# Performance work log

Measured on AMD Instinct MI355X. Metric: run time of the kernel, lower is better.

Reference implementation:

```python
import jax, jax.numpy as jnp
import numpy as np

B, S, D, H = 4, 2048, 256, 8  # batch, seq (context=target), hidden_dim, n_heads


def setup_inputs() -> dict:
    key = jax.random.key(0)
    ks = jax.random.split(key, 12)
    sd = 1.0 / np.sqrt(D)          # torch Linear default init scale (uniform bound)
    sdo = 1.0 / np.sqrt(H * D)
    inp = {
        "k": jax.random.normal(ks[0], (B, S, D), jnp.float32),
        "v": jax.random.normal(ks[1], (B, S, D), jnp.float32),
        "q": jax.random.normal(ks[2], (B, S, D), jnp.float32),
        # Per-head projection weights, stacked over heads. Stored so y = x @ W + b.
        "Wk": jax.random.uniform(ks[3], (H, D, D), jnp.float32, -sd, sd),
        "bk": jax.random.uniform(ks[4], (H, D), jnp.float32, -sd, sd),
        "Wv": jax.random.uniform(ks[5], (H, D, D), jnp.float32, -sd, sd),
        "bv": jax.random.uniform(ks[6], (H, D), jnp.float32, -sd, sd),
        "Wq": jax.random.uniform(ks[7], (H, D, D), jnp.float32, -sd, sd),
        "bq": jax.random.uniform(ks[8], (H, D), jnp.float32, -sd, sd),
        # Final mixing Linear: input is heads interleaved as (hidden, head) flattened,
        # i.e. input index = hid * H + head (torch stack(dim=-1).view order).
        "Wo": jax.random.uniform(ks[9], (H * D, D), jnp.float32, -sdo, sdo),
        "bo": jax.random.uniform(ks[10], (D,), jnp.float32, -sdo, sdo),
    }
    return inp


def reference(k, v, q, Wk, bk, Wv, bv, Wq, bq, Wo, bo):
    # Per-head linear projections (batched over heads instead of a Python loop)
    k_ = jnp.einsum('bmd,hde->bhme', k, Wk) + bk[None, :, None, :]  # [B,H,S,D]
    v_ = jnp.einsum('bmd,hde->bhme', v, Wv) + bv[None, :, None, :]
    q_ = jnp.einsum('bnd,hde->bhne', q, Wq) + bq[None, :, None, :]
    scale = jnp.asarray(np.sqrt(D), k.dtype)
    # dot attention: scores[b,h,n,m] = <q_n, k_m> / sqrt(D); softmax over keys m
    scores = jnp.einsum('bhnd,bhmd->bhnm', q_, k_) / scale
    w = jax.nn.softmax(scores, axis=-1)
    rep = jnp.einsum('bhnm,bhmd->bhnd', w, v_)  # [B,H,S,D]
    # torch: stack(heads, dim=-1) -> [B,S,D,H], then view -> [B,S,D*H] (hid-major)
    outs = rep.transpose(0, 2, 3, 1).reshape(rep.shape[0], rep.shape[2], -1)
    return outs @ Wo + bo
```

## Files before the change

kernel.cpp:

```cpp
#include <hip/hip_runtime.h>

#define BB 4
#define SS 2048
#define DD 256
#define HH 8

typedef unsigned short u16;
typedef __attribute__((ext_vector_type(8))) short bf16x8;
typedef __attribute__((ext_vector_type(4))) float f32x4;
typedef __attribute__((ext_vector_type(16))) float f32x16;
typedef __attribute__((ext_vector_type(4))) short s16x4;

__device__ __forceinline__ f32x4 MFMA(bf16x8 a, bf16x8 b, f32x4 c) {
    return __builtin_amdgcn_mfma_f32_16x16x32_bf16(a, b, c, 0, 0, 0);
}
__device__ __forceinline__ f32x16 MFMA32(bf16x8 a, bf16x8 b, f32x16 c) {
    return __builtin_amdgcn_mfma_f32_32x32x16_bf16(a, b, c, 0, 0, 0);
}

__device__ __forceinline__ u16 f2bf_rtn(float x) {
    unsigned u = __float_as_uint(x);
    u += 0x7FFFu + ((u >> 16) & 1u);
    return (u16)(u >> 16);
}
__device__ __forceinline__ float bf2f(u16 h) {
    return __uint_as_float(((unsigned)h) << 16);
}
__device__ __forceinline__ void split2(float x, u16 &hi, u16 &lo) {
    hi = f2bf_rtn(x);
    lo = f2bf_rtn(x - bf2f(hi));
}

__device__ __forceinline__ void gl_lds16(const u16* g, u16* l) {
    __builtin_amdgcn_global_load_lds(
        (const __attribute__((address_space(1))) unsigned int*)(g),
        (__attribute__((address_space(3))) unsigned int*)(l), 16, 0, 0);
}

__global__ void prep_a(const float* __restrict__ x, u16* __restrict__ hi) {
    int r = blockIdx.x;
    int d = threadIdx.x;
    hi[(size_t)r * 256 + d] = f2bf_rtn(x[(size_t)r * 256 + d]);
}

__global__ void prep_w(const float* __restrict__ W, u16* __restrict__ Whi,
                       u16* __restrict__ Wlo) {
    int n = blockIdx.x;
    int h = n >> 8, e = n & 255;
    int d = threadIdx.x;
    float x = W[((size_t)h * 256 + d) * 256 + e];
    u16 hi, lo; split2(x, hi, lo);
    Whi[(size_t)n * 256 + d] = hi;
    Wlo[(size_t)n * 256 + d] = lo;
}

__global__ void prep_wo(const float* __restrict__ W, u16* __restrict__ Whi,
                        u16* __restrict__ Wlo) {
    int n = blockIdx.x;
    for (int k = threadIdx.x; k < 2048; k += 256) {
        int d = k & 255, h = k >> 8;
        float x = W[((size_t)(d * 8 + h)) * 256 + n];
        u16 hi, lo; split2(x, hi, lo);
        Whi[(size_t)n * 2048 + k] = hi;
        Wlo[(size_t)n * 2048 + k] = lo;
    }
}

template<int MODE, int AMODE, int TERMS, int BN>
__global__ __launch_bounds__(512, 2) void gemm_split(
    const u16* __restrict__ Ahi, const u16* __restrict__ Alo,
    const u16* __restrict__ Bhi, const u16* __restrict__ Blo,
    const float* __restrict__ bias,
    u16* __restrict__ Ohi,
    float* __restrict__ Of,
    int M, int N, int K, float scale)
{
    constexpr int WN = (BN == 128) ? 4 : 2;
    constexpr int WM = 8 / WN;
    constexpr int MSUB = (128 / WM) / 16;
    constexpr int NSUB = (BN / WN) / 16;
    constexpr int NPL = (TERMS == 3) ? 4 : (TERMS == 2) ? 3 : 2;

    __shared__ u16 lds[3 * NPL * 4096];

    const int tid = threadIdx.x;
    const int lane = tid & 63, wave = tid >> 6;
    const int wm = wave / WN, wn = wave % WN;
    const int m0 = blockIdx.y * 128, n0 = blockIdx.x * BN;

    f32x4 acc[MSUB][NSUB];
#pragma unroll
    for (int i = 0; i < MSUB; ++i)
#pragma unroll
        for (int j = 0; j < NSUB; ++j) acc[i][j] = {0.f, 0.f, 0.f, 0.f};

    const int rho = tid >> 2;
    const int Xs = (tid & 3) << 3;
    const int ldsW = wave * 512;

#define G_ISSUE(k0v, p)                                                         \
    {   u16* Bse = lds + (p) * (NPL * 4096);                                    \
        size_t ga;                                                              \
        if (AMODE == 0)                                                         \
            ga = (size_t)(m0 + rho) * K + (k0v) + Xs;                           \
        else                                                                    \
            ga = ((size_t)((m0 >> 11) * 8 + ((k0v) >> 8)) * SS                  \
                  + (m0 & 2047) + rho) * DD + ((k0v) & 255) + Xs;               \
        gl_lds16(Ahi + ga, Bse + ldsW);                                         \
        if (TERMS == 3) gl_lds16(Alo + ga, Bse + 3 * 4096 + ldsW);              \
        if (BN == 128 || tid < 256) {                                           \
            size_t gb = (size_t)(n0 + rho) * K + (k0v) + Xs;                    \
            gl_lds16(Bhi + gb, Bse + 1 * 4096 + ldsW);                          \
            if (TERMS >= 2) gl_lds16(Blo + gb, Bse + 2 * 4096 + ldsW);          \
        }                                                                       \
    }

    const int NK = K >> 5;
    G_ISSUE(0, 0);
    G_ISSUE(32, 1);

    int buf = 0;
    for (int kt = 0; kt < NK; ++kt) {
        if (kt < NK - 1) {
            if (TERMS == 1)      { asm volatile("s_waitcnt vmcnt(2)" ::: "memory"); }
            else if (TERMS == 2) { asm volatile("s_waitcnt vmcnt(3)" ::: "memory"); }
            else {
                if (wave < 4) { asm volatile("s_waitcnt vmcnt(4)" ::: "memory"); }
                else          { asm volatile("s_waitcnt vmcnt(2)" ::: "memory"); }
            }
        } else {
            asm volatile("s_waitcnt vmcnt(0)" ::: "memory");
        }
        __builtin_amdgcn_sched_barrier(0);
        __builtin_amdgcn_s_barrier();
        __builtin_amdgcn_sched_barrier(0);

        if (kt + 2 < NK) {
            const int p2 = (buf + 2 >= 3) ? buf - 1 : buf + 2;
            G_ISSUE((kt + 2) << 5, p2);
        }

        const u16* Bse = lds + buf * (NPL * 4096);
        const int g8 = (lane >> 4) << 3;
        const int rA = wm * (128 / WM), rB = wn * (BN / WN);
        bf16x8 bh[NSUB], bl[NSUB];
#pragma unroll
        for (int ns = 0; ns < NSUB; ++ns) {
            const int rb = rB + ns * 16 + (lane & 15);
            bh[ns] = *(const bf16x8*)(Bse + 1 * 4096 + rb * 32 + g8);
            if (TERMS >= 2) bl[ns] = *(const bf16x8*)(Bse + 2 * 4096 + rb * 32 + g8);
        }
#pragma unroll
        for (int ms = 0; ms < MSUB; ++ms) {
            const int ra = rA + ms * 16 + (lane & 15);
            bf16x8 ah = *(const bf16x8*)(Bse + ra * 32 + g8);
            bf16x8 al;
            if (TERMS == 3) al = *(const bf16x8*)(Bse + 3 * 4096 + ra * 32 + g8);
#pragma unroll
            for (int ns = 0; ns < NSUB; ++ns) {
                acc[ms][ns] = MFMA(ah, bh[ns], acc[ms][ns]);
                if (TERMS == 3) acc[ms][ns] = MFMA(al, bh[ns], acc[ms][ns]);
                if (TERMS >= 2) acc[ms][ns] = MFMA(ah, bl[ns], acc[ms][ns]);
            }
        }
        buf = (buf + 1 == 3) ? 0 : buf + 1;
    }
#undef G_ISSUE

#pragma unroll
    for (int ms = 0; ms < MSUB; ++ms)
#pragma unroll
        for (int ns = 0; ns < NSUB; ++ns)
#pragma unroll
            for (int r = 0; r < 4; ++r) {
                int row = m0 + wm * (128 / WM) + ms * 16 + (lane >> 4) * 4 + r;
                int col = n0 + wn * (BN / WN) + ns * 16 + (lane & 15);
                float v = (acc[ms][ns][r] + bias[col]) * scale;
                if (MODE == 2) {
                    Of[(size_t)row * N + col] = v;
                } else {
                    int b = row >> 11, s = row & 2047, hh = col >> 8, e = col & 255;
                    size_t idx;
                    if (MODE == 0)
                        idx = ((size_t)(b * HH + hh) * SS + s) * DD + e;
                    else
                        idx = ((size_t)(b * HH + hh) * DD + e) * SS + s;
                    Ohi[idx] = f2bf_rtn(v);
                }
            }
}

__global__ __launch_bounds__(512, 2) void attn_kernel(
    const u16* __restrict__ Qhi,
    const u16* __restrict__ Khi,
    const u16* __restrict__ Vhi,
    u16* __restrict__ Rhi, u16* __restrict__ Rlo)
{
    __shared__ u16 lK[3][8192];
    __shared__ u16 lV[3][8192];

    const int tid = threadIdx.x, lane = tid & 63, wave = tid >> 6;
    const int qc = lane & 31, g2 = lane >> 5;
    const int wg = ((blockIdx.x & 7) << 5) + (blockIdx.x >> 3);
    const int bh = wg >> 3;
    const int qt = wg & 7;
    const size_t base = (size_t)bh * SS * DD;
    const int q0w = qt * 256 + wave * 32;

    bf16x8 qB[16];
#pragma unroll
    for (int ks = 0; ks < 16; ++ks)
        qB[ks] = *(const bf16x8*)(Qhi + base + (size_t)(q0w + qc) * DD + ks * 16 + g2 * 8);

    int koff[2], voff[2];
#pragma unroll
    for (int i = 0; i < 2; ++i) {
        const int s = tid + i * 512;
        const int kr = s >> 5, kX = s & 31;
        const int kap = (kr & 0x13) | ((kr & 4) << 1) | ((kr & 8) >> 1);
        koff[i] = kap * DD + ((kX ^ kr) << 3);
        const int ve = s >> 2, vXs = s & 3;
        voff[i] = ve * SS + (((vXs ^ ((ve >> 3) & 3))) << 3);
    }

    float l_part = 0.f;
    f32x16 acc[8];
#pragma unroll
    for (int ec = 0; ec < 8; ++ec) acc[ec] = {};

#define ISSUE(tt, p)                                                            \
    {   const u16* Kg = Khi + base + (size_t)(tt) * 32 * DD;                    \
        const u16* Vg = Vhi + base + (size_t)(tt) * 32;                         \
        u16* Kb = &lK[p][0]; u16* Vb = &lV[p][0];                               \
        gl_lds16(Kg + koff[0], Kb + wave * 512);                                \
        gl_lds16(Kg + koff[1], Kb + wave * 512 + 4096);                         \
        gl_lds16(Vg + voff[0], Vb + wave * 512);                                \
        gl_lds16(Vg + voff[1], Vb + wave * 512 + 4096);                         \
    }

    ISSUE(0, 0);
    ISSUE(1, 1);

    for (int t = 0; t < 64; ++t) {
        if (t < 63) { asm volatile("s_waitcnt vmcnt(4)" ::: "memory"); }
        else        { asm volatile("s_waitcnt vmcnt(0)" ::: "memory"); }
        __builtin_amdgcn_sched_barrier(0);
        __builtin_amdgcn_s_barrier();
        __builtin_amdgcn_sched_barrier(0);

        if (t + 2 < 64) ISSUE(t + 2, (t + 2) % 3);

        const u16* Kb = &lK[t % 3][0];
        const u16* Vb = &lV[t % 3][0];

        f32x16 sa = {}, sb = {};
        __builtin_amdgcn_s_setprio(1);
#pragma unroll
        for (int ks = 0; ks < 8; ++ks) {
            bf16x8 ka = *(const bf16x8*)(Kb + qc * DD + (((2 * ks + g2) ^ qc) << 3));
            bf16x8 kb2 = *(const bf16x8*)(Kb + qc * DD + (((2 * (ks + 8) + g2) ^ qc) << 3));
            sa = MFMA32(ka, qB[ks], sa);
            sb = MFMA32(kb2, qB[ks + 8], sb);
        }
        __builtin_amdgcn_s_setprio(0);

        f32x16 s = sa + sb;
#pragma unroll
        for (int n = 0; n < 16; ++n) s[n] = __builtin_amdgcn_exp2f(s[n] - 8.0f);
        float tl = 0.f;
#pragma unroll
        for (int n = 0; n < 16; ++n) tl += s[n];
        l_part += tl;

        bf16x8 p0, p1;
#pragma unroll
        for (int j = 0; j < 8; ++j) p0[j] = (short)f2bf_rtn(s[j]);
#pragma unroll
        for (int j = 0; j < 8; ++j) p1[j] = (short)f2bf_rtn(s[8 + j]);

        __builtin_amdgcn_s_setprio(1);
#pragma unroll
        for (int ec = 0; ec < 8; ++ec) {
            const int e = ec * 32 + qc;
            bf16x8 v0 = *(const bf16x8*)(Vb + e * 32 + (((g2 ^ ((e >> 3) & 3))) << 3));
            bf16x8 v1 = *(const bf16x8*)(Vb + e * 32 + ((((2 + g2) ^ ((e >> 3) & 3))) << 3));
            acc[ec] = MFMA32(v0, p0, acc[ec]);
            acc[ec] = MFMA32(v1, p1, acc[ec]);
        }
        __builtin_amdgcn_s_setprio(0);
    }
#undef ISSUE

    float l = l_part + __shfl_xor(l_part, 32);
    float inv = 1.0f / l;
    const size_t rowbase = ((size_t)bh * SS + q0w + qc) * DD;
#pragma unroll
    for (int ec = 0; ec < 8; ++ec)
#pragma unroll
        for (int rr = 0; rr < 4; ++rr) {
            const int e0 = ec * 32 + 8 * rr + 4 * g2;
            s16x4 hv, lv;
#pragma unroll
            for (int j = 0; j < 4; ++j) {
                u16 h2, l2; split2(acc[ec][4 * rr + j] * inv, h2, l2);
                hv[j] = (short)h2; lv[j] = (short)l2;
            }
            *(s16x4*)(Rhi + rowbase + e0) = hv;
            *(s16x4*)(Rlo + rowbase + e0) = lv;
        }
}

extern "C" void kernel_launch(void* const* d_in, const int* in_sizes, int n_in,
                              void* d_out, int out_size, void* d_ws, size_t ws_size,
                              hipStream_t stream)
{
    (void)in_sizes; (void)n_in; (void)out_size; (void)ws_size;
    const float* k_in = (const float*)d_in[0];
    const float* v_in = (const float*)d_in[1];
    const float* q_in = (const float*)d_in[2];
    const float* Wk   = (const float*)d_in[3];
    const float* bk   = (const float*)d_in[4];
    const float* Wv   = (const float*)d_in[5];
    const float* bv   = (const float*)d_in[6];
    const float* Wq   = (const float*)d_in[7];
    const float* bq   = (const float*)d_in[8];
    const float* Wo   = (const float*)d_in[9];
    const float* bo   = (const float*)d_in[10];
    float* out = (float*)d_out;

    char* p = (char*)d_ws;
    const size_t MB = 1024 * 1024;
    u16* WqH = (u16*)(p + 0 * MB);
    u16* WqL = (u16*)(p + 1 * MB);
    u16* WkH = (u16*)(p + 2 * MB);
    u16* WkL = (u16*)(p + 3 * MB);
    u16* WvH = (u16*)(p + 4 * MB);
    u16* WvL = (u16*)(p + 5 * MB);
    u16* WoH = (u16*)(p + 6 * MB);
    u16* WoL = (u16*)(p + 7 * MB);
    const size_t PB = 32 * MB;
    u16* QH  = (u16*)(p + 8 * MB);
    u16* KH  = (u16*)(p + 8 * MB + 1 * PB);
    u16* VTH = (u16*)(p + 8 * MB + 2 * PB);
    u16* RH  = (u16*)(p + 8 * MB + 3 * PB);
    u16* RL  = (u16*)(p + 8 * MB + 4 * PB);
    u16* AqH = (u16*)(p + 168 * MB);
    u16* AkH = (u16*)(p + 172 * MB);
    u16* AvH = (u16*)(p + 176 * MB);

    prep_a<<<dim3(8192), dim3(256), 0, stream>>>(q_in, AqH);
    prep_a<<<dim3(8192), dim3(256), 0, stream>>>(k_in, AkH);
    prep_a<<<dim3(8192), dim3(256), 0, stream>>>(v_in, AvH);
    prep_w<<<dim3(2048), dim3(256), 0, stream>>>(Wq, WqH, WqL);
    prep_w<<<dim3(2048), dim3(256), 0, stream>>>(Wk, WkH, WkL);
    prep_w<<<dim3(2048), dim3(256), 0, stream>>>(Wv, WvH, WvL);
    prep_wo<<<dim3(256), dim3(256), 0, stream>>>(Wo, WoH, WoL);

    const float qscale = 1.4426950408889634f / 16.0f;
    gemm_split<0, 0, 1, 128><<<dim3(16, 64), dim3(512), 0, stream>>>(
        AqH, nullptr, WqH, WqL, bq, QH, nullptr, 8192, 2048, 256, qscale);
    gemm_split<0, 0, 1, 128><<<dim3(16, 64), dim3(512), 0, stream>>>(
        AkH, nullptr, WkH, WkL, bk, KH, nullptr, 8192, 2048, 256, 1.0f);
    gemm_split<1, 0, 2, 128><<<dim3(16, 64), dim3(512), 0, stream>>>(
        AvH, nullptr, WvH, WvL, bv, VTH, nullptr, 8192, 2048, 256, 1.0f);

    attn_kernel<<<dim3(256), dim3(512), 0, stream>>>(
        QH, KH, VTH, RH, RL);

    gemm_split<2, 2, 3, 64><<<dim3(4, 64), dim3(512), 0, stream>>>(
        RH, RL, WoH, WoL, bo, nullptr, out, 8192, 256, 2048, 1.0f);
}
```

Baseline: 309.6 us.

## Halve attention workgroup size to double grid, remap GEMM blocks XCD-aware

```diff
diff --git a/kernel.cpp b/kernel.cpp
--- a/kernel.cpp
+++ b/kernel.cpp
@@ -66,7 +66,7 @@
     }
 }
 
-template<int MODE, int AMODE, int TERMS, int BN>
+template<int MODE, int AMODE, int TERMS, int BN, int LNXB>
 __global__ __launch_bounds__(512, 2) void gemm_split(
     const u16* __restrict__ Ahi, const u16* __restrict__ Alo,
     const u16* __restrict__ Bhi, const u16* __restrict__ Blo,
@@ -86,7 +86,10 @@
     const int tid = threadIdx.x;
     const int lane = tid & 63, wave = tid >> 6;
     const int wm = wave / WN, wn = wave % WN;
-    const int m0 = blockIdx.y * 128, n0 = blockIdx.x * BN;
+    const int cpx = (int)gridDim.x >> 3;
+    const int wgs = (blockIdx.x & 7) * cpx + (blockIdx.x >> 3);
+    const int m0 = (wgs >> LNXB) * 128;
+    const int n0 = (wgs & ((1 << LNXB) - 1)) * BN;
 
     f32x4 acc[MSUB][NSUB];
 #pragma unroll
@@ -190,32 +193,32 @@
             }
 }
 
-__global__ __launch_bounds__(512, 2) void attn_kernel(
+__global__ __launch_bounds__(256, 2) void attn_kernel(
     const u16* __restrict__ Qhi,
     const u16* __restrict__ Khi,
     const u16* __restrict__ Vhi,
     u16* __restrict__ Rhi, u16* __restrict__ Rlo)
 {
-    __shared__ u16 lK[3][8192];
-    __shared__ u16 lV[3][8192];
+    __shared__ u16 lK[2][8192];
+    __shared__ u16 lV[2][8192];
 
     const int tid = threadIdx.x, lane = tid & 63, wave = tid >> 6;
     const int qc = lane & 31, g2 = lane >> 5;
-    const int wg = ((blockIdx.x & 7) << 5) + (blockIdx.x >> 3);
-    const int bh = wg >> 3;
-    const int qt = wg & 7;
+    const int wg = ((blockIdx.x & 7) << 6) + (blockIdx.x >> 3);
+    const int bh = wg >> 4;
+    const int qt = wg & 15;
     const size_t base = (size_t)bh * SS * DD;
-    const int q0w = qt * 256 + wave * 32;
+    const int q0w = qt * 128 + wave * 32;
 
     bf16x8 qB[16];
 #pragma unroll
     for (int ks = 0; ks < 16; ++ks)
         qB[ks] = *(const bf16x8*)(Qhi + base + (size_t)(q0w + qc) * DD + ks * 16 + g2 * 8);
 
-    int koff[2], voff[2];
-#pragma unroll
-    for (int i = 0; i < 2; ++i) {
-        const int s = tid + i * 512;
+    int koff[4], voff[4];
+#pragma unroll
+    for (int i = 0; i < 4; ++i) {
+        const int s = wave * 256 + i * 64 + lane;
         const int kr = s >> 5, kX = s & 31;
         const int kap = (kr & 0x13) | ((kr & 4) << 1) | ((kr & 8) >> 1);
         koff[i] = kap * DD + ((kX ^ kr) << 3);
@@ -231,27 +234,26 @@
 #define ISSUE(tt, p)                                                            \
     {   const u16* Kg = Khi + base + (size_t)(tt) * 32 * DD;                    \
         const u16* Vg = Vhi + base + (size_t)(tt) * 32;                         \
-        u16* Kb = &lK[p][0]; u16* Vb = &lV[p][0];                               \
-        gl_lds16(Kg + koff[0], Kb + wave * 512);                                \
-        gl_lds16(Kg + koff[1], Kb + wave * 512 + 4096);                         \
-        gl_lds16(Vg + voff[0], Vb + wave * 512);                                \
-        gl_lds16(Vg + voff[1], Vb + wave * 512 + 4096);                         \
+        u16* Kb_ = &lK[p][0]; u16* Vb_ = &lV[p][0];                             \
+        _Pragma("unroll")                                                       \
+        for (int i = 0; i < 4; ++i) {                                           \
+            gl_lds16(Kg + koff[i], Kb_ + (wave * 4 + i) * 512);                 \
+            gl_lds16(Vg + voff[i], Vb_ + (wave * 4 + i) * 512);                 \
+        }                                                                       \
     }
 
     ISSUE(0, 0);
-    ISSUE(1, 1);
 
     for (int t = 0; t < 64; ++t) {
-        if (t < 63) { asm volatile("s_waitcnt vmcnt(4)" ::: "memory"); }
-        else        { asm volatile("s_waitcnt vmcnt(0)" ::: "memory"); }
+        asm volatile("s_waitcnt vmcnt(0)" ::: "memory");
         __builtin_amdgcn_sched_barrier(0);
         __builtin_amdgcn_s_barrier();
         __builtin_amdgcn_sched_barrier(0);
 
-        if (t + 2 < 64) ISSUE(t + 2, (t + 2) % 3);
-
-        const u16* Kb = &lK[t % 3][0];
-        const u16* Vb = &lV[t % 3][0];
+        if (t + 1 < 64) ISSUE(t + 1, (t + 1) & 1);
+
+        const u16* Kb = &lK[t & 1][0];
+        const u16* Vb = &lV[t & 1][0];
 
         f32x16 sa = {}, sb = {};
         __builtin_amdgcn_s_setprio(1);
@@ -357,16 +359,16 @@
     prep_wo<<<dim3(256), dim3(256), 0, stream>>>(Wo, WoH, WoL);
 
     const float qscale = 1.4426950408889634f / 16.0f;
-    gemm_split<0, 0, 1, 128><<<dim3(16, 64), dim3(512), 0, stream>>>(
+    gemm_split<0, 0, 1, 128, 4><<<dim3(1024), dim3(512), 0, stream>>>(
         AqH, nullptr, WqH, WqL, bq, QH, nullptr, 8192, 2048, 256, qscale);
-    gemm_split<0, 0, 1, 128><<<dim3(16, 64), dim3(512), 0, stream>>>(
+    gemm_split<0, 0, 1, 128, 4><<<dim3(1024), dim3(512), 0, stream>>>(
         AkH, nullptr, WkH, WkL, bk, KH, nullptr, 8192, 2048, 256, 1.0f);
-    gemm_split<1, 0, 2, 128><<<dim3(16, 64), dim3(512), 0, stream>>>(
+    gemm_split<1, 0, 2, 128, 4><<<dim3(1024), dim3(512), 0, stream>>>(
         AvH, nullptr, WvH, WvL, bv, VTH, nullptr, 8192, 2048, 256, 1.0f);
 
-    attn_kernel<<<dim3(256), dim3(512), 0, stream>>>(
+    attn_kernel<<<dim3(512), dim3(256), 0, stream>>>(
         QH, KH, VTH, RH, RL);
 
-    gemm_split<2, 2, 3, 64><<<dim3(4, 64), dim3(512), 0, stream>>>(
+    gemm_split<2, 2, 3, 64, 2><<<dim3(256), dim3(512), 0, stream>>>(
         RH, RL, WoH, WoL, bo, nullptr, out, 8192, 256, 2048, 1.0f);
 }
```

After: 308.4 us. About the same (-0.4%).
